# Kernel tuning notes

Hardware: AMD Instinct MI355X
Metric: run time of the kernel (lower is better)

Reference implementation:

```python
import jax, jax.numpy as jnp
import numpy as np

N_NODES = 50000
N_EDGES = 600000
N_FEAT = 64
D = 128
N_GRAPHS = 1024
N_LAYERS = 4


def setup_inputs() -> dict:
    key = jax.random.key(0)
    ks = jax.random.split(key, 16)
    x = jax.random.normal(ks[0], (N_NODES, N_FEAT), dtype=jnp.float32)
    edge_index = jax.random.randint(ks[1], (2, N_EDGES), 0, N_NODES, dtype=jnp.int64)
    batch_index = jnp.sort(jax.random.randint(ks[2], (N_NODES,), 0, N_GRAPHS, dtype=jnp.int64))
    def lin(k, fan_in, fan_out):
        s = 1.0 / np.sqrt(fan_in)
        kw, kb = jax.random.split(k)
        w = jax.random.uniform(kw, (fan_in, fan_out), minval=-s, maxval=s, dtype=jnp.float32)
        b = jax.random.uniform(kb, (fan_out,), minval=-s, maxval=s, dtype=jnp.float32)
        return w, b
    w0, b0 = lin(ks[3], N_FEAT, D)
    w1, b1 = lin(ks[4], D, D)
    w2, b2 = lin(ks[5], D, D)
    w3, b3 = lin(ks[6], D, D)
    wp, bp = lin(ks[7], D, D)
    return {"x": x, "edge_index": edge_index, "batch_index": batch_index,
            "w0": w0, "b0": b0, "w1": w1, "b1": b1, "w2": w2, "b2": b2,
            "w3": w3, "b3": b3, "wp": wp, "bp": bp}


def _gin_layer(x, src, dst, w, b):
    # GINConv with eps=0: MLP(x_i + sum_{j in N(i)} x_j); MLP = Linear -> ReLU
    agg = jax.ops.segment_sum(x[src], dst, num_segments=N_NODES)
    return jax.nn.relu((x + agg) @ w + b)


def reference(x, edge_index, batch_index, w0, b0, w1, b1, w2, b2, w3, b3, wp, bp):
    src, dst = edge_index[0], edge_index[1]
    # first layer changes width 64 -> 128; agg happens in input width
    agg0 = jax.ops.segment_sum(x[src], dst, num_segments=N_NODES)
    h = jax.nn.relu((x + agg0) @ w0 + b0)
    for w, b in ((w1, b1), (w2, b2), (w3, b3)):
        h = _gin_layer(h, src, dst, w, b)
    # global mean pool per graph
    sums = jax.ops.segment_sum(h, batch_index, num_segments=N_GRAPHS)
    counts = jax.ops.segment_sum(jnp.ones((N_NODES,), dtype=h.dtype), batch_index, num_segments=N_GRAPHS)
    pooled = sums / jnp.maximum(counts, 1.0)[:, None]
    # post_mp: Linear -> ReLU (dropout identity at inference)
    return jax.nn.relu(pooled @ wp + bp)
```

## Files before the change

### kernel.cpp

```cpp
#include <hip/hip_runtime.h>
#include <hip/hip_fp16.h>


#define N_NODES  50000
#define N_EDGES  600000
#define N_FEAT   64
#define DIM      128
#define N_GRAPHS 1024
#define NC       7
#define CSH      13
#define TOT2     (N_NODES * NC)
#define SCH      2048
#define NBLK     ((TOT2 + SCH - 1) / SCH)
#define TPB      256
#define GT32     ((N_NODES + 31) / 32)

typedef _Float16 f16x8 __attribute__((ext_vector_type(8)));
typedef float    f32x4 __attribute__((ext_vector_type(4)));

#define CNTZ2 (TOT2 / 4)
#define XWORK (N_NODES * N_FEAT / 4)
#define PREP_TOTAL (CNTZ2 + XWORK + N_FEAT * DIM + 3 * DIM * DIM)

__global__ __launch_bounds__(TPB) void prep_k(
    const float* __restrict__ x, __half* __restrict__ xh,
    const float* __restrict__ w0, const float* __restrict__ w1,
    const float* __restrict__ w2, const float* __restrict__ w3,
    __half* __restrict__ Wt0, __half* __restrict__ Wt1,
    __half* __restrict__ Wt2, __half* __restrict__ Wt3,
    int* __restrict__ cnt2) {
  int i = blockIdx.x * TPB + threadIdx.x;
  if (i < CNTZ2) {
    *reinterpret_cast<int4*>(cnt2 + i * 4) = make_int4(0, 0, 0, 0);
    return;
  }
  i -= CNTZ2;
  if (i < XWORK) {
    float4 v = *reinterpret_cast<const float4*>(x + (size_t)i * 4);
    union { __half2 h2[2]; uint2 u; } pk;
    pk.h2[0] = __floats2half2_rn(v.x, v.y);
    pk.h2[1] = __floats2half2_rn(v.z, v.w);
    *reinterpret_cast<uint2*>(xh + (size_t)i * 4) = pk.u;
    return;
  }
  int j = i - XWORK;
  if (j < N_FEAT * DIM) {
    int k = j >> 7, n = j & 127;
    Wt0[n * N_FEAT + k] = __float2half(w0[j]);
    return;
  }
  j -= N_FEAT * DIM;
  if (j >= 3 * DIM * DIM) return;
  int wsel = j / (DIM * DIM);
  int jj = j - wsel * (DIM * DIM);
  int k = jj >> 7, n = jj & 127;
  const float* W = (wsel == 0) ? w1 : (wsel == 1) ? w2 : w3;
  __half* Wt     = (wsel == 0) ? Wt1 : (wsel == 1) ? Wt2 : Wt3;
  Wt[n * DIM + k] = __float2half(W[jj]);
}

__global__ __launch_bounds__(TPB) void hist_k(
    const int* __restrict__ src, const int* __restrict__ dst,
    int* __restrict__ cnt2, int* __restrict__ rank) {
  int e = blockIdx.x * TPB + threadIdx.x;
  if (e >= N_EDGES) return;
  int key = dst[e] * NC + (src[e] >> CSH);
  rank[e] = atomicAdd(&cnt2[key], 1);
}

__global__ __launch_bounds__(TPB) void scan_part_k(
    const int* __restrict__ cnt2, int* __restrict__ part) {
  __shared__ int ws[4];
  int t = threadIdx.x, b = blockIdx.x;
  int base = b * SCH + t * 8;
  int s = 0;
  if (base < TOT2) {
    int4 a = *reinterpret_cast<const int4*>(cnt2 + base);
    int4 c = *reinterpret_cast<const int4*>(cnt2 + base + 4);
    s = a.x + a.y + a.z + a.w + c.x + c.y + c.z + c.w;
  }
  for (int off = 32; off; off >>= 1) s += __shfl_down(s, off, 64);
  int lane = t & 63, wv = t >> 6;
  if (lane == 0) ws[wv] = s;
  __syncthreads();
  if (t == 0) part[b] = ws[0] + ws[1] + ws[2] + ws[3];
}

__global__ __launch_bounds__(TPB) void scan_write_k(
    const int* __restrict__ cnt2, const int* __restrict__ part,
    int* __restrict__ row_ptr2) {
  __shared__ int pscan[TPB];
  __shared__ int wsum[4];
  int t = threadIdx.x, b = blockIdx.x;
  int lane = t & 63, wv = t >> 6;
  int base = b * SCH + t * 8;

  pscan[t] = (t < NBLK) ? part[t] : 0;
  __syncthreads();
  for (int off = 1; off < TPB; off <<= 1) {
    int v = (t >= off) ? pscan[t - off] : 0;
    __syncthreads();
    pscan[t] += v;
    __syncthreads();
  }
  int blk_off = (b > 0) ? pscan[b - 1] : 0;

  int v[8] = {0,0,0,0,0,0,0,0};
  if (base < TOT2) {
    int4 a = *reinterpret_cast<const int4*>(cnt2 + base);
    int4 c = *reinterpret_cast<const int4*>(cnt2 + base + 4);
    v[0]=a.x; v[1]=a.y; v[2]=a.z; v[3]=a.w;
    v[4]=c.x; v[5]=c.y; v[6]=c.z; v[7]=c.w;
  }
  int ls = 0;
#pragma unroll
  for (int i = 0; i < 8; ++i) ls += v[i];
  int incl = ls;
  for (int off = 1; off < 64; off <<= 1) {
    int u = __shfl_up(incl, off, 64);
    if (lane >= off) incl += u;
  }
  if (lane == 63) wsum[wv] = incl;
  __syncthreads();
  int woff = 0;
  for (int w = 0; w < wv; ++w) woff += wsum[w];
  int run = blk_off + woff + (incl - ls);
  if (base < TOT2) {
    int rp[8];
#pragma unroll
    for (int i = 0; i < 8; ++i) { rp[i] = run; run += v[i]; }
    *reinterpret_cast<int4*>(row_ptr2 + base) = make_int4(rp[0], rp[1], rp[2], rp[3]);
    *reinterpret_cast<int4*>(row_ptr2 + base + 4) = make_int4(rp[4], rp[5], rp[6], rp[7]);
  }
  if (b == 0 && t == 0) row_ptr2[TOT2] = N_EDGES;
}

__global__ __launch_bounds__(TPB) void fill_k(
    const int* __restrict__ src, const int* __restrict__ dst,
    const int* __restrict__ row_ptr2, const int* __restrict__ rank,
    int* __restrict__ csr_src) {
  int e = blockIdx.x * TPB + threadIdx.x;
  if (e >= N_EDGES) return;
  int s = src[e];
  int key = dst[e] * NC + (s >> CSH);
  csr_src[row_ptr2[key] + rank[e]] = s;
}

template<int F, bool BR>
__global__ __launch_bounds__(TPB) void gather_k(
    const __half* __restrict__ y, const int* __restrict__ row_ptr2,
    const int* __restrict__ csr_src, const float* __restrict__ bias,
    __half* __restrict__ hout) {
  constexpr int CH = F / 8;
  const f16x8* yv = reinterpret_cast<const f16x8*>(y);
  int gid  = blockIdx.x * TPB + threadIdx.x;
  int node = gid / CH;
  int l    = gid % CH;
  if (node >= N_NODES) return;
  int beg = row_ptr2[node * NC];
  int end = row_ptr2[node * NC + NC];

  f16x8 self = yv[(size_t)node * CH + l];
  float acc[8];
#pragma unroll
  for (int v = 0; v < 8; ++v) acc[v] = (float)self[v];

  int e = beg;
  for (; e + 3 < end; e += 4) {
    int s0 = csr_src[e+0], s1 = csr_src[e+1], s2 = csr_src[e+2], s3 = csr_src[e+3];
    f16x8 v0 = yv[(size_t)s0 * CH + l];
    f16x8 v1 = yv[(size_t)s1 * CH + l];
    f16x8 v2 = yv[(size_t)s2 * CH + l];
    f16x8 v3 = yv[(size_t)s3 * CH + l];
#pragma unroll
    for (int v = 0; v < 8; ++v)
      acc[v] += ((float)v0[v] + (float)v1[v]) + ((float)v2[v] + (float)v3[v]);
  }
  for (; e < end; ++e) {
    f16x8 v0 = yv[(size_t)csr_src[e] * CH + l];
#pragma unroll
    for (int v = 0; v < 8; ++v) acc[v] += (float)v0[v];
  }

  f16x8 o;
  if (BR) {
    float4 b0 = *reinterpret_cast<const float4*>(bias + l * 8);
    float4 b1 = *reinterpret_cast<const float4*>(bias + l * 8 + 4);
    float bb[8] = {b0.x, b0.y, b0.z, b0.w, b1.x, b1.y, b1.z, b1.w};
#pragma unroll
    for (int v = 0; v < 8; ++v) o[v] = (_Float16)fmaxf(acc[v] + bb[v], 0.f);
  } else {
#pragma unroll
    for (int v = 0; v < 8; ++v) o[v] = (_Float16)acc[v];
  }
  reinterpret_cast<f16x8*>(hout)[(size_t)node * CH + l] = o;
}

__global__ __launch_bounds__(TPB) void gg00_k(
    const __half* __restrict__ s, const __half* __restrict__ Wt0,
    const float* __restrict__ b0, const __half* __restrict__ Wt1,
    __half* __restrict__ y1) {
  __shared__ __align__(16) __half As[32][72];
  __shared__ __align__(16) __half Hs[32][136];
  int tid = threadIdx.x;
  int row0 = blockIdx.x * 32;

  {
    int r = tid >> 3, c = (tid & 7) * 8;
    int row = min(row0 + r, N_NODES - 1);
    *reinterpret_cast<f16x8*>(&As[r][c]) =
        *reinterpret_cast<const f16x8*>(s + (size_t)row * N_FEAT + c);
  }
  __syncthreads();

  int w = tid >> 6, lane = tid & 63;
  int quad = lane >> 4, m = lane & 15;
  int col0 = w * 32;

  f32x4 accA[2][2];
#pragma unroll
  for (int mt = 0; mt < 2; ++mt)
#pragma unroll
    for (int nt = 0; nt < 2; ++nt) accA[mt][nt] = (f32x4){0.f,0.f,0.f,0.f};
#pragma unroll
  for (int kc = 0; kc < 2; ++kc) {
    f16x8 a0 = *reinterpret_cast<const f16x8*>(&As[m][kc*32 + quad*8]);
    f16x8 a1 = *reinterpret_cast<const f16x8*>(&As[16 + m][kc*32 + quad*8]);
#pragma unroll
    for (int nt = 0; nt < 2; ++nt) {
      f16x8 b = *reinterpret_cast<const f16x8*>(
          Wt0 + (size_t)(col0 + nt*16 + m) * N_FEAT + kc*32 + quad*8);
      accA[0][nt] = __builtin_amdgcn_mfma_f32_16x16x32_f16(a0, b, accA[0][nt], 0, 0, 0);
      accA[1][nt] = __builtin_amdgcn_mfma_f32_16x16x32_f16(a1, b, accA[1][nt], 0, 0, 0);
    }
  }
#pragma unroll
  for (int mt = 0; mt < 2; ++mt)
#pragma unroll
    for (int nt = 0; nt < 2; ++nt) {
      float bv = b0[col0 + nt*16 + m];
#pragma unroll
      for (int r = 0; r < 4; ++r)
        Hs[mt*16 + quad*4 + r][col0 + nt*16 + m] =
            __float2half(fmaxf(accA[mt][nt][r] + bv, 0.f));
    }
  __syncthreads();

  f32x4 accB[2][2];
#pragma unroll
  for (int mt = 0; mt < 2; ++mt)
#pragma unroll
    for (int nt = 0; nt < 2; ++nt) accB[mt][nt] = (f32x4){0.f,0.f,0.f,0.f};
#pragma unroll
  for (int kc = 0; kc < 4; ++kc) {
    f16x8 a0 = *reinterpret_cast<const f16x8*>(&Hs[m][kc*32 + quad*8]);
    f16x8 a1 = *reinterpret_cast<const f16x8*>(&Hs[16 + m][kc*32 + quad*8]);
#pragma unroll
    for (int nt = 0; nt < 2; ++nt) {
      f16x8 b = *reinterpret_cast<const f16x8*>(
          Wt1 + (size_t)(col0 + nt*16 + m) * DIM + kc*32 + quad*8);
      accB[0][nt] = __builtin_amdgcn_mfma_f32_16x16x32_f16(a0, b, accB[0][nt], 0, 0, 0);
      accB[1][nt] = __builtin_amdgcn_mfma_f32_16x16x32_f16(a1, b, accB[1][nt], 0, 0, 0);
    }
  }
  __syncthreads();
#pragma unroll
  for (int mt = 0; mt < 2; ++mt)
#pragma unroll
    for (int nt = 0; nt < 2; ++nt)
#pragma unroll
      for (int r = 0; r < 4; ++r)
        Hs[mt*16 + quad*4 + r][col0 + nt*16 + m] = __float2half(accB[mt][nt][r]);
  __syncthreads();
#pragma unroll
  for (int it = 0; it < 2; ++it) {
    int i = tid + it * TPB;
    int r = i >> 4, c = (i & 15) * 8;
    int row = row0 + r;
    if (row < N_NODES)
      *reinterpret_cast<f16x8*>(y1 + (size_t)row * DIM + c) =
          *reinterpret_cast<const f16x8*>(&Hs[r][c]);
  }
}

__global__ __launch_bounds__(TPB) void fgg_k(
    const __half* __restrict__ y, const int* __restrict__ row_ptr2,
    const int* __restrict__ csr_src, const float* __restrict__ bias,
    const __half* __restrict__ Wn, __half* __restrict__ yout) {
  __shared__ __align__(16) __half As[32][136];
  const f16x8* yv = reinterpret_cast<const f16x8*>(y);
  int tid = threadIdx.x;
  int row0 = blockIdx.x * 32;
  int g = tid >> 4, l = tid & 15;

#pragma unroll 1
  for (int p = 0; p < 2; ++p) {
    int node = row0 + p * 16 + g;
    if (node < N_NODES) {
      int beg = row_ptr2[node * NC];
      int end = row_ptr2[node * NC + NC];
      f16x8 self = yv[(size_t)node * 16 + l];
      float acc[8];
#pragma unroll
      for (int v = 0; v < 8; ++v) acc[v] = (float)self[v];
      int e = beg;
      for (; e + 3 < end; e += 4) {
        int s0 = csr_src[e+0], s1 = csr_src[e+1], s2 = csr_src[e+2], s3 = csr_src[e+3];
        f16x8 v0 = yv[(size_t)s0 * 16 + l];
        f16x8 v1 = yv[(size_t)s1 * 16 + l];
        f16x8 v2 = yv[(size_t)s2 * 16 + l];
        f16x8 v3 = yv[(size_t)s3 * 16 + l];
#pragma unroll
        for (int v = 0; v < 8; ++v)
          acc[v] += ((float)v0[v] + (float)v1[v]) + ((float)v2[v] + (float)v3[v]);
      }
      for (; e < end; ++e) {
        f16x8 v0 = yv[(size_t)csr_src[e] * 16 + l];
#pragma unroll
        for (int v = 0; v < 8; ++v) acc[v] += (float)v0[v];
      }
      float4 bb0 = *reinterpret_cast<const float4*>(bias + l * 8);
      float4 bb1 = *reinterpret_cast<const float4*>(bias + l * 8 + 4);
      float bb[8] = {bb0.x, bb0.y, bb0.z, bb0.w, bb1.x, bb1.y, bb1.z, bb1.w};
      f16x8 o;
#pragma unroll
      for (int v = 0; v < 8; ++v) o[v] = (_Float16)fmaxf(acc[v] + bb[v], 0.f);
      *reinterpret_cast<f16x8*>(&As[p * 16 + g][l * 8]) = o;
    }
  }
  __syncthreads();

  int w = tid >> 6, lane = tid & 63;
  int quad = lane >> 4, m = lane & 15;
  int col0 = w * 32;
  f32x4 acc2[2][2];
#pragma unroll
  for (int mt = 0; mt < 2; ++mt)
#pragma unroll
    for (int nt = 0; nt < 2; ++nt) acc2[mt][nt] = (f32x4){0.f,0.f,0.f,0.f};
#pragma unroll
  for (int kc = 0; kc < 4; ++kc) {
    f16x8 a0 = *reinterpret_cast<const f16x8*>(&As[m][kc*32 + quad*8]);
    f16x8 a1 = *reinterpret_cast<const f16x8*>(&As[16 + m][kc*32 + quad*8]);
#pragma unroll
    for (int nt = 0; nt < 2; ++nt) {
      f16x8 b = *reinterpret_cast<const f16x8*>(
          Wn + (size_t)(col0 + nt*16 + m) * DIM + kc*32 + quad*8);
      acc2[0][nt] = __builtin_amdgcn_mfma_f32_16x16x32_f16(a0, b, acc2[0][nt], 0, 0, 0);
      acc2[1][nt] = __builtin_amdgcn_mfma_f32_16x16x32_f16(a1, b, acc2[1][nt], 0, 0, 0);
    }
  }
  __syncthreads();
#pragma unroll
  for (int mt = 0; mt < 2; ++mt)
#pragma unroll
    for (int nt = 0; nt < 2; ++nt)
#pragma unroll
      for (int r = 0; r < 4; ++r)
        As[mt*16 + quad*4 + r][col0 + nt*16 + m] = __float2half(acc2[mt][nt][r]);
  __syncthreads();
#pragma unroll
  for (int it = 0; it < 2; ++it) {
    int i = tid + it * TPB;
    int r = i >> 4, c = (i & 15) * 8;
    int row = row0 + r;
    if (row < N_NODES)
      *reinterpret_cast<f16x8*>(yout + (size_t)row * DIM + c) =
          *reinterpret_cast<const f16x8*>(&As[r][c]);
  }
}

__global__ __launch_bounds__(128) void pool_post_k(
    const __half* __restrict__ h, const int* __restrict__ batch,
    const float* __restrict__ W, const float* __restrict__ bias,
    float* __restrict__ out) {
  __shared__ float xs[DIM];
  int g = blockIdx.x;
  int col = threadIdx.x;
  int lo = 0, hi = N_NODES;
  while (lo < hi) { int mid = (lo + hi) >> 1; if (batch[mid] < g) lo = mid + 1; else hi = mid; }
  int beg = lo;
  hi = N_NODES;
  while (lo < hi) { int mid = (lo + hi) >> 1; if (batch[mid] < g + 1) lo = mid + 1; else hi = mid; }
  int end = lo;

  float acc = 0.f;
  for (int n = beg; n < end; ++n) acc += __half2float(h[(size_t)n * DIM + col]);
  float cnt = fmaxf((float)(end - beg), 1.0f);
  xs[col] = acc / cnt;
  __syncthreads();
  float o = bias[col];
  for (int k = 0; k < DIM; ++k)
    o = fmaf(xs[k], W[(size_t)k * DIM + col], o);
  out[(size_t)g * DIM + col] = fmaxf(o, 0.f);
}

extern "C" void kernel_launch(void* const* d_in, const int* in_sizes, int n_in,
                              void* d_out, int out_size, void* d_ws, size_t ws_size,
                              hipStream_t stream) {
  const float* x    = (const float*)d_in[0];
  const int*   ei   = (const int*)d_in[1];
  const int*   batch= (const int*)d_in[2];
  const float* w0 = (const float*)d_in[3];  const float* b0 = (const float*)d_in[4];
  const float* w1 = (const float*)d_in[5];  const float* b1 = (const float*)d_in[6];
  const float* w2 = (const float*)d_in[7];  const float* b2 = (const float*)d_in[8];
  const float* w3 = (const float*)d_in[9];  const float* b3 = (const float*)d_in[10];
  const float* wp = (const float*)d_in[11]; const float* bp = (const float*)d_in[12];
  float* out = (float*)d_out;

  const int* src = ei;
  const int* dst = ei + N_EDGES;

  __half* xh = (__half*)d_ws;
  __half* sb = xh + (size_t)N_NODES * N_FEAT;
  __half* yA = sb + (size_t)N_NODES * N_FEAT;
  __half* yB = yA + (size_t)N_NODES * DIM;
  __half* h  = yB + (size_t)N_NODES * DIM;
  __half* Wt0 = h + (size_t)N_NODES * DIM;
  __half* Wt1 = Wt0 + N_FEAT * DIM;
  __half* Wt2 = Wt1 + DIM * DIM;
  __half* Wt3 = Wt2 + DIM * DIM;
  int* cnt2     = (int*)(Wt3 + DIM * DIM);
  int* rank     = cnt2 + TOT2;
  int* part     = rank + N_EDGES;
  int* row_ptr2 = part + 256;
  int* csr_src  = row_ptr2 + (TOT2 + 1);

  prep_k<<<(PREP_TOTAL + TPB - 1) / TPB, TPB, 0, stream>>>(
      x, xh, w0, w1, w2, w3, Wt0, Wt1, Wt2, Wt3, cnt2);
  hist_k<<<(N_EDGES + TPB - 1) / TPB, TPB, 0, stream>>>(src, dst, cnt2, rank);
  scan_part_k <<<NBLK, TPB, 0, stream>>>(cnt2, part);
  scan_write_k<<<NBLK, TPB, 0, stream>>>(cnt2, part, row_ptr2);
  fill_k<<<(N_EDGES + TPB - 1) / TPB, TPB, 0, stream>>>(src, dst, row_ptr2,
                                                        rank, csr_src);

  gather_k<N_FEAT, false><<<(N_NODES * 8 + TPB - 1) / TPB, TPB, 0, stream>>>(
      xh, row_ptr2, csr_src, nullptr, sb);

  gg00_k<<<GT32, TPB, 0, stream>>>(sb, Wt0, b0, Wt1, yA);

  fgg_k<<<GT32, TPB, 0, stream>>>(yA, row_ptr2, csr_src, b1, Wt2, yB);
  fgg_k<<<GT32, TPB, 0, stream>>>(yB, row_ptr2, csr_src, b2, Wt3, yA);

  gather_k<DIM, true><<<(N_NODES * 16 + TPB - 1) / TPB, TPB, 0, stream>>>(
      yA, row_ptr2, csr_src, b3, h);

  pool_post_k<<<N_GRAPHS, 128, 0, stream>>>(h, batch, wp, bp, out);
}
```

Measured before the change: 263.3 us.

## Fuse first aggregation into GEMM and final aggregation into atomic pooling

```diff
diff --git a/kernel.cpp b/kernel.cpp
--- a/kernel.cpp
+++ b/kernel.cpp
@@ -19,8 +19,9 @@
 typedef float    f32x4 __attribute__((ext_vector_type(4)));
 
 #define CNTZ2 (TOT2 / 4)
+#define PSZ4  (N_GRAPHS * DIM / 4)
 #define XWORK (N_NODES * N_FEAT / 4)
-#define PREP_TOTAL (CNTZ2 + XWORK + N_FEAT * DIM + 3 * DIM * DIM)
+#define PREP_TOTAL (CNTZ2 + PSZ4 + XWORK + N_FEAT * DIM + 3 * DIM * DIM)
 
 __global__ __launch_bounds__(TPB) void prep_k(
     const float* __restrict__ x, __half* __restrict__ xh,
@@ -28,13 +29,18 @@
     const float* __restrict__ w2, const float* __restrict__ w3,
     __half* __restrict__ Wt0, __half* __restrict__ Wt1,
     __half* __restrict__ Wt2, __half* __restrict__ Wt3,
-    int* __restrict__ cnt2) {
+    int* __restrict__ cnt2, int* __restrict__ pool_sums) {
   int i = blockIdx.x * TPB + threadIdx.x;
   if (i < CNTZ2) {
     *reinterpret_cast<int4*>(cnt2 + i * 4) = make_int4(0, 0, 0, 0);
     return;
   }
   i -= CNTZ2;
+  if (i < PSZ4) {
+    *reinterpret_cast<int4*>(pool_sums + i * 4) = make_int4(0, 0, 0, 0);
+    return;
+  }
+  i -= PSZ4;
   if (i < XWORK) {
     float4 v = *reinterpret_cast<const float4*>(x + (size_t)i * 4);
     union { __half2 h2[2]; uint2 u; } pk;
@@ -146,70 +152,51 @@
   csr_src[row_ptr2[key] + rank[e]] = s;
 }
 
-template<int F, bool BR>
-__global__ __launch_bounds__(TPB) void gather_k(
-    const __half* __restrict__ y, const int* __restrict__ row_ptr2,
-    const int* __restrict__ csr_src, const float* __restrict__ bias,
-    __half* __restrict__ hout) {
-  constexpr int CH = F / 8;
-  const f16x8* yv = reinterpret_cast<const f16x8*>(y);
-  int gid  = blockIdx.x * TPB + threadIdx.x;
-  int node = gid / CH;
-  int l    = gid % CH;
-  if (node >= N_NODES) return;
-  int beg = row_ptr2[node * NC];
-  int end = row_ptr2[node * NC + NC];
-
-  f16x8 self = yv[(size_t)node * CH + l];
-  float acc[8];
-#pragma unroll
-  for (int v = 0; v < 8; ++v) acc[v] = (float)self[v];
-
-  int e = beg;
-  for (; e + 3 < end; e += 4) {
-    int s0 = csr_src[e+0], s1 = csr_src[e+1], s2 = csr_src[e+2], s3 = csr_src[e+3];
-    f16x8 v0 = yv[(size_t)s0 * CH + l];
-    f16x8 v1 = yv[(size_t)s1 * CH + l];
-    f16x8 v2 = yv[(size_t)s2 * CH + l];
-    f16x8 v3 = yv[(size_t)s3 * CH + l];
-#pragma unroll
-    for (int v = 0; v < 8; ++v)
-      acc[v] += ((float)v0[v] + (float)v1[v]) + ((float)v2[v] + (float)v3[v]);
-  }
-  for (; e < end; ++e) {
-    f16x8 v0 = yv[(size_t)csr_src[e] * CH + l];
-#pragma unroll
-    for (int v = 0; v < 8; ++v) acc[v] += (float)v0[v];
-  }
-
-  f16x8 o;
-  if (BR) {
-    float4 b0 = *reinterpret_cast<const float4*>(bias + l * 8);
-    float4 b1 = *reinterpret_cast<const float4*>(bias + l * 8 + 4);
-    float bb[8] = {b0.x, b0.y, b0.z, b0.w, b1.x, b1.y, b1.z, b1.w};
-#pragma unroll
-    for (int v = 0; v < 8; ++v) o[v] = (_Float16)fmaxf(acc[v] + bb[v], 0.f);
-  } else {
-#pragma unroll
-    for (int v = 0; v < 8; ++v) o[v] = (_Float16)acc[v];
-  }
-  reinterpret_cast<f16x8*>(hout)[(size_t)node * CH + l] = o;
-}
-
-__global__ __launch_bounds__(TPB) void gg00_k(
-    const __half* __restrict__ s, const __half* __restrict__ Wt0,
-    const float* __restrict__ b0, const __half* __restrict__ Wt1,
-    __half* __restrict__ y1) {
+__global__ __launch_bounds__(TPB) void g64gg_k(
+    const __half* __restrict__ xh, const int* __restrict__ row_ptr2,
+    const int* __restrict__ csr_src,
+    const __half* __restrict__ Wt0, const float* __restrict__ b0,
+    const __half* __restrict__ Wt1, __half* __restrict__ y1) {
   __shared__ __align__(16) __half As[32][72];
   __shared__ __align__(16) __half Hs[32][136];
+  const f16x8* xv = reinterpret_cast<const f16x8*>(xh);
   int tid = threadIdx.x;
   int row0 = blockIdx.x * 32;
 
   {
-    int r = tid >> 3, c = (tid & 7) * 8;
-    int row = min(row0 + r, N_NODES - 1);
-    *reinterpret_cast<f16x8*>(&As[r][c]) =
-        *reinterpret_cast<const f16x8*>(s + (size_t)row * N_FEAT + c);
+    int ns = tid >> 3, l = tid & 7;
+    int node = row0 + ns;
+    f16x8 o;
+    if (node < N_NODES) {
+      int beg = row_ptr2[node * NC];
+      int end = row_ptr2[node * NC + NC];
+      f16x8 self = xv[(size_t)node * 8 + l];
+      float acc[8];
+#pragma unroll
+      for (int v = 0; v < 8; ++v) acc[v] = (float)self[v];
+      int e = beg;
+      for (; e + 3 < end; e += 4) {
+        int s0 = csr_src[e+0], s1 = csr_src[e+1], s2 = csr_src[e+2], s3 = csr_src[e+3];
+        f16x8 v0 = xv[(size_t)s0 * 8 + l];
+        f16x8 v1 = xv[(size_t)s1 * 8 + l];
+        f16x8 v2 = xv[(size_t)s2 * 8 + l];
+        f16x8 v3 = xv[(size_t)s3 * 8 + l];
+#pragma unroll
+        for (int v = 0; v < 8; ++v)
+          acc[v] += ((float)v0[v] + (float)v1[v]) + ((float)v2[v] + (float)v3[v]);
+      }
+      for (; e < end; ++e) {
+        f16x8 v0 = xv[(size_t)csr_src[e] * 8 + l];
+#pragma unroll
+        for (int v = 0; v < 8; ++v) acc[v] += (float)v0[v];
+      }
+#pragma unroll
+      for (int v = 0; v < 8; ++v) o[v] = (_Float16)acc[v];
+    } else {
+#pragma unroll
+      for (int v = 0; v < 8; ++v) o[v] = (_Float16)0.f;
+    }
+    *reinterpret_cast<f16x8*>(&As[ns][l * 8]) = o;
   }
   __syncthreads();
 
@@ -370,8 +357,52 @@
   }
 }
 
-__global__ __launch_bounds__(128) void pool_post_k(
-    const __half* __restrict__ h, const int* __restrict__ batch,
+__global__ __launch_bounds__(TPB) void gpool_k(
+    const __half* __restrict__ y, const int* __restrict__ row_ptr2,
+    const int* __restrict__ csr_src, const float* __restrict__ bias,
+    const int* __restrict__ batch, float* __restrict__ pool_sums) {
+  const f16x8* yv = reinterpret_cast<const f16x8*>(y);
+  int gid  = blockIdx.x * TPB + threadIdx.x;
+  int node = gid / 16;
+  int l    = gid % 16;
+  if (node >= N_NODES) return;
+  int beg = row_ptr2[node * NC];
+  int end = row_ptr2[node * NC + NC];
+
+  f16x8 self = yv[(size_t)node * 16 + l];
+  float acc[8];
+#pragma unroll
+  for (int v = 0; v < 8; ++v) acc[v] = (float)self[v];
+
+  int e = beg;
+  for (; e + 3 < end; e += 4) {
+    int s0 = csr_src[e+0], s1 = csr_src[e+1], s2 = csr_src[e+2], s3 = csr_src[e+3];
+    f16x8 v0 = yv[(size_t)s0 * 16 + l];
+    f16x8 v1 = yv[(size_t)s1 * 16 + l];
+    f16x8 v2 = yv[(size_t)s2 * 16 + l];
+    f16x8 v3 = yv[(size_t)s3 * 16 + l];
+#pragma unroll
+    for (int v = 0; v < 8; ++v)
+      acc[v] += ((float)v0[v] + (float)v1[v]) + ((float)v2[v] + (float)v3[v]);
+  }
+  for (; e < end; ++e) {
+    f16x8 v0 = yv[(size_t)csr_src[e] * 16 + l];
+#pragma unroll
+    for (int v = 0; v < 8; ++v) acc[v] += (float)v0[v];
+  }
+
+  float4 b0 = *reinterpret_cast<const float4*>(bias + l * 8);
+  float4 b1 = *reinterpret_cast<const float4*>(bias + l * 8 + 4);
+  float bb[8] = {b0.x, b0.y, b0.z, b0.w, b1.x, b1.y, b1.z, b1.w};
+  int g = batch[node];
+  float* ps = pool_sums + (size_t)g * DIM + l * 8;
+#pragma unroll
+  for (int v = 0; v < 8; ++v)
+    atomicAdd(ps + v, fmaxf(acc[v] + bb[v], 0.f));
+}
+
+__global__ __launch_bounds__(128) void post_k(
+    const float* __restrict__ pool_sums, const int* __restrict__ batch,
     const float* __restrict__ W, const float* __restrict__ bias,
     float* __restrict__ out) {
   __shared__ float xs[DIM];
@@ -384,10 +415,8 @@
   while (lo < hi) { int mid = (lo + hi) >> 1; if (batch[mid] < g + 1) lo = mid + 1; else hi = mid; }
   int end = lo;
 
-  float acc = 0.f;
-  for (int n = beg; n < end; ++n) acc += __half2float(h[(size_t)n * DIM + col]);
   float cnt = fmaxf((float)(end - beg), 1.0f);
-  xs[col] = acc / cnt;
+  xs[col] = pool_sums[(size_t)g * DIM + col] / cnt;
   __syncthreads();
   float o = bias[col];
   for (int k = 0; k < DIM; ++k)
@@ -412,38 +441,33 @@
   const int* dst = ei + N_EDGES;
 
   __half* xh = (__half*)d_ws;
-  __half* sb = xh + (size_t)N_NODES * N_FEAT;
-  __half* yA = sb + (size_t)N_NODES * N_FEAT;
+  __half* yA = xh + (size_t)N_NODES * N_FEAT;
   __half* yB = yA + (size_t)N_NODES * DIM;
-  __half* h  = yB + (size_t)N_NODES * DIM;
-  __half* Wt0 = h + (size_t)N_NODES * DIM;
+  __half* Wt0 = yB + (size_t)N_NODES * DIM;
   __half* Wt1 = Wt0 + N_FEAT * DIM;
   __half* Wt2 = Wt1 + DIM * DIM;
   __half* Wt3 = Wt2 + DIM * DIM;
-  int* cnt2     = (int*)(Wt3 + DIM * DIM);
+  float* pool_sums = (float*)(Wt3 + DIM * DIM);
+  int* cnt2     = (int*)(pool_sums + N_GRAPHS * DIM);
   int* rank     = cnt2 + TOT2;
   int* part     = rank + N_EDGES;
   int* row_ptr2 = part + 256;
   int* csr_src  = row_ptr2 + (TOT2 + 1);
 
   prep_k<<<(PREP_TOTAL + TPB - 1) / TPB, TPB, 0, stream>>>(
-      x, xh, w0, w1, w2, w3, Wt0, Wt1, Wt2, Wt3, cnt2);
+      x, xh, w0, w1, w2, w3, Wt0, Wt1, Wt2, Wt3, cnt2, (int*)pool_sums);
   hist_k<<<(N_EDGES + TPB - 1) / TPB, TPB, 0, stream>>>(src, dst, cnt2, rank);
   scan_part_k <<<NBLK, TPB, 0, stream>>>(cnt2, part);
   scan_write_k<<<NBLK, TPB, 0, stream>>>(cnt2, part, row_ptr2);
   fill_k<<<(N_EDGES + TPB - 1) / TPB, TPB, 0, stream>>>(src, dst, row_ptr2,
                                                         rank, csr_src);
 
-  gather_k<N_FEAT, false><<<(N_NODES * 8 + TPB - 1) / TPB, TPB, 0, stream>>>(
-      xh, row_ptr2, csr_src, nullptr, sb);
-
-  gg00_k<<<GT32, TPB, 0, stream>>>(sb, Wt0, b0, Wt1, yA);
+  g64gg_k<<<GT32, TPB, 0, stream>>>(xh, row_ptr2, csr_src, Wt0, b0, Wt1, yA);
 
   fgg_k<<<GT32, TPB, 0, stream>>>(yA, row_ptr2, csr_src, b1, Wt2, yB);
   fgg_k<<<GT32, TPB, 0, stream>>>(yB, row_ptr2, csr_src, b2, Wt3, yA);
 
-  gather_k<DIM, true><<<(N_NODES * 16 + TPB - 1) / TPB, TPB, 0, stream>>>(
-      yA, row_ptr2, csr_src, b3, h);
-
-  pool_post_k<<<N_GRAPHS, 128, 0, stream>>>(h, batch, wp, bp, out);
-}
+  gpool_k<<<(N_NODES * 16 + TPB - 1) / TPB, TPB, 0, stream>>>(
+      yA, row_ptr2, csr_src, b3, batch, pool_sums);
+  post_k<<<N_GRAPHS, 128, 0, stream>>>(pool_sums, batch, wp, bp, out);
+}
```

Result: slower. 449.3 us (+70.7%).
